# Kernel optimization log

Measured on AMD Instinct MI355X. Metric: run time of the kernel, lower is better.

The kernel has to match this reference:

```python
import jax, jax.numpy as jnp
import numpy as np

H = 2048      # hidden_dim
DI = 4096     # intermediate_size
N = 128       # state_size
NH = 64       # num_heads
P = 64        # head_dim
K = 4         # conv kernel
CH = 256      # chunk size
L = 4096      # seq len
DT_MIN, DT_MAX = 1e-3, 1e2


def setup_inputs() -> dict:
    key = jax.random.key(0)
    ks = jax.random.split(key, 8)
    conv_dim = DI + 2 * N
    x = jax.random.normal(ks[0], (L, H), jnp.float32)
    W_in = jax.random.normal(ks[1], (DI + 2 * N + NH, H), jnp.float32) / np.sqrt(H)
    conv_w = jax.random.normal(ks[2], (conv_dim, 1, K), jnp.float32) / np.sqrt(K)
    conv_b = jax.random.normal(ks[3], (conv_dim,), jnp.float32) * 0.01
    u = jax.random.uniform(ks[4], (NH,))
    dt = jnp.exp(u * (np.log(0.1) - np.log(0.001)) + np.log(0.001))
    dt = jnp.maximum(dt, 1e-4)
    dt_bias = dt + jnp.log(-jnp.expm1(-dt))   # inverse-softplus init
    A_log = jnp.log(jax.random.uniform(ks[5], (NH,), minval=1.0, maxval=16.0))
    D = jnp.ones((NH,), jnp.float32)
    norm_w = jnp.ones((DI,), jnp.float32)
    W_out = jax.random.normal(ks[6], (H, DI), jnp.float32) / np.sqrt(DI)
    return dict(x=x, W_in=W_in, conv_w=conv_w, conv_b=conv_b, dt_bias=dt_bias,
                A_log=A_log, D=D, norm_w=norm_w, W_out=W_out)


def _causal_decay(a):
    # a: [..., T] per-step log-decays -> exp(segment sum) as lower-tri [..., T, T]
    T = a.shape[-1]
    strict = jnp.tril(jnp.ones((T, T), bool), -1)
    full = jnp.tril(jnp.ones((T, T), bool), 0)
    s = jnp.cumsum(jnp.where(strict, a[..., None], 0.0), axis=-2)
    return jnp.where(full, jnp.exp(s), 0.0)


def reference(x, W_in, conv_w, conv_b, dt_bias, A_log, D, norm_w, W_out):
    conv_dim = DI + 2 * N
    xBCdt = x @ W_in.T                                  # [L, DI+2N+NH]
    xBC, dt = xBCdt[:, :conv_dim], xBCdt[:, conv_dim:]
    # causal depthwise conv1d + SiLU
    z = jax.lax.conv_general_dilated(
        xBC.T[None], conv_w, (1,), [(K - 1, 0)],
        dimension_numbers=('NCH', 'OIH', 'NCH'),
        feature_group_count=conv_dim)[0] + conv_b[:, None]
    xBC = jax.nn.silu(z.T)                              # [L, conv_dim]
    x_ssm = xBC[:, :DI].reshape(L, NH, P)
    Bm = xBC[:, DI:DI + N]                              # [L, N] shared over heads
    Cm = xBC[:, DI + N:]                                # [L, N]
    dt = jnp.clip(jax.nn.softplus(dt + dt_bias), DT_MIN, DT_MAX)  # [L, NH]
    A = -jnp.exp(A_log.astype(jnp.float32))             # [NH]
    dA = dt * A                                         # [L, NH]
    xdt = x_ssm * dt[:, :, None]                        # [L, NH, P]
    nc = L // CH
    xc = xdt.reshape(nc, CH, NH, P)
    Bc = Bm.reshape(nc, CH, N)
    Cc = Cm.reshape(nc, CH, N)
    dAc = dA.reshape(nc, CH, NH)
    A_cs = jnp.cumsum(dAc, axis=1)                      # [c, k, h]
    # intra-chunk (diagonal blocks)
    Lmat = _causal_decay(dAc.transpose(0, 2, 1))        # [c, h, k, k]
    Y_diag = jnp.einsum('ckn,csn,chks,cshp->ckhp', Cc, Bc, Lmat, xc)
    # per-chunk right states
    decay_states = jnp.exp(A_cs[:, -1:, :] - A_cs)      # [c, k, h]
    states = jnp.einsum('ckn,ckh,ckhp->chpn', Bc, decay_states, xc)
    # inter-chunk recurrence (no initial state)
    chunk_sum = A_cs[:, -1, :].T                        # [h, c]
    dec = _causal_decay(jnp.pad(chunk_sum, ((0, 0), (1, 0))))  # [h, c+1, c+1]
    states = jnp.concatenate([jnp.zeros((1, NH, P, N), states.dtype), states], 0)
    new_states = jnp.einsum('hzc,chpn->zhpn', dec, states)      # [c+1, h, p, n]
    prev = new_states[:-1]                              # [c, h, p, n]
    Y_off = jnp.einsum('ckn,chpn,ckh->ckhp', Cc, prev, jnp.exp(A_cs))
    Y = (Y_diag + Y_off).reshape(L, NH, P) + x_ssm * D[None, :, None]
    y = Y.reshape(L, DI)
    # RMSNorm
    var = jnp.mean(jnp.square(y.astype(jnp.float32)), -1, keepdims=True)
    y = (y * jax.lax.rsqrt(var + 1e-6)) * norm_w
    return y @ W_out.T
```

## Files before the change

### kernel.cpp

```cpp
#include <hip/hip_runtime.h>


typedef __bf16 bf16;
typedef __bf16 bf16x8 __attribute__((ext_vector_type(8)));
typedef __bf16 bf16x4 __attribute__((ext_vector_type(4)));
typedef float  f32x4  __attribute__((ext_vector_type(4)));

#define DEV static __device__ __forceinline__

DEV f32x4 mfma16(bf16x8 a, bf16x8 b, f32x4 c) {
  return __builtin_amdgcn_mfma_f32_16x16x32_bf16(a, b, c, 0, 0, 0);
}

DEV void gll16(const bf16* g, bf16* l) {
  __builtin_amdgcn_global_load_lds(
      (const __attribute__((address_space(1))) unsigned int*)g,
      (__attribute__((address_space(3))) unsigned int*)l, 16, 0, 0);
}

#define BAR()   asm volatile("s_barrier" ::: "memory")
#define VMW(n)  asm volatile("s_waitcnt vmcnt(" #n ")" ::: "memory")

template <int NT, int LD, bool DTC>
__global__ __launch_bounds__(512) void gemm_kernel(
    const bf16* __restrict__ Abase, const bf16* __restrict__ Bbase,
    bf16* __restrict__ C0, bf16* __restrict__ C1,
    float* __restrict__ dt0, float* __restrict__ dt1, int ldc, int ntN) {
  __shared__ __align__(16) bf16 lds[2 * 32768];
  const int tid = threadIdx.x;
  const int wid = tid >> 6, lane = tid & 63;
  const int lrow = lane & 15;
  const int colb = (lane >> 4) * 16;
  const int xorv = (lrow & 7) << 4;
  const int wm = wid & 1, wn = wid >> 1;
  const int bx = blockIdx.x / ntN, by = blockIdx.x % ntN;
  const int row0 = bx * 256, col0 = by * 256;
  const bf16* A = Abase + (size_t)blockIdx.y * (NT * 64);
  const bf16* B = Bbase + (size_t)blockIdx.y * (NT * 64);
  bf16* C = blockIdx.y ? C1 : C0;

  const int P = tid * 16;
  const int Lc = P ^ (((P >> 7) & 7) << 4);
  const int srow = Lc >> 7;
  const int selem = (Lc & 127) >> 1;
  const bf16* gA[4];
  const bf16* gB[4];
#pragma unroll
  for (int q = 0; q < 4; ++q) {
    gA[q] = A + (size_t)(row0 + q * 64 + srow) * LD + selem;
    gB[q] = B + (size_t)(col0 + q * 64 + srow) * LD + selem;
  }
  auto stage = [&](int s, int ko) {
#pragma unroll
    for (int q = 0; q < 4; ++q)
      gll16(gA[q] + ko, lds + s * 32768 + q * 4096 + tid * 8);
#pragma unroll
    for (int q = 0; q < 4; ++q)
      gll16(gB[q] + ko, lds + s * 32768 + 16384 + q * 4096 + tid * 8);
  };
  auto rdA = [&](int s, int m, int ks) -> bf16x8 {
    int row = wm * 128 + m * 16 + lrow;
    int cb = ((ks << 6) | colb) ^ xorv;
    return *(const bf16x8*)((const char*)(lds + s * 32768) + row * 128 + cb);
  };
  auto rdB = [&](int s, int n, int ks) -> bf16x8 {
    int row = wn * 64 + n * 16 + lrow;
    int cb = ((ks << 6) | colb) ^ xorv;
    return *(const bf16x8*)((const char*)(lds + s * 32768 + 16384) + row * 128 + cb);
  };

  f32x4 acc[8][4] = {};
  bf16x8 aF[4][2], bF[4][2];

  stage(0, 0);
  VMW(0);
  BAR();

  for (int t = 0; t < NT; ++t) {
    const int s = t & 1;
    if (t + 1 < NT) stage(s ^ 1, (t + 1) * 64);
#pragma unroll
    for (int n = 0; n < 4; ++n)
#pragma unroll
      for (int ks = 0; ks < 2; ++ks) bF[n][ks] = rdB(s, n, ks);
#pragma unroll
    for (int m = 0; m < 4; ++m)
#pragma unroll
      for (int ks = 0; ks < 2; ++ks) aF[m][ks] = rdA(s, m, ks);
#pragma unroll
    for (int m = 0; m < 4; ++m)
#pragma unroll
      for (int n = 0; n < 4; ++n)
#pragma unroll
        for (int ks = 0; ks < 2; ++ks)
          acc[m][n] = mfma16(aF[m][ks], bF[n][ks], acc[m][n]);
#pragma unroll
    for (int m = 0; m < 4; ++m)
#pragma unroll
      for (int ks = 0; ks < 2; ++ks) aF[m][ks] = rdA(s, m + 4, ks);
#pragma unroll
    for (int m = 0; m < 4; ++m)
#pragma unroll
      for (int n = 0; n < 4; ++n)
#pragma unroll
        for (int ks = 0; ks < 2; ++ks)
          acc[m + 4][n] = mfma16(aF[m][ks], bF[n][ks], acc[m + 4][n]);
    if (t + 1 < NT) {
      VMW(0);
      BAR();
    }
  }
  const int orow = (lane >> 4) * 4;
#pragma unroll
  for (int m = 0; m < 8; ++m)
#pragma unroll
    for (int n = 0; n < 4; ++n)
#pragma unroll
      for (int i = 0; i < 4; ++i) {
        int r = row0 + wm * 128 + m * 16 + orow + i;
        int c = col0 + wn * 64 + n * 16 + lrow;
        C[(size_t)r * ldc + c] = (bf16)acc[m][n][i];
      }
  if (DTC && by == 17 && wn == 0) {
    float* dtp = blockIdx.y ? dt1 : dt0;
#pragma unroll
    for (int m = 0; m < 8; ++m)
#pragma unroll
      for (int n = 0; n < 4; ++n)
#pragma unroll
        for (int i = 0; i < 4; ++i) {
          int r = row0 + wm * 128 + m * 16 + orow + i;
          int h = n * 16 + lrow;
          dtp[(size_t)r * 64 + h] = acc[m][n][i];
        }
  }
}

__global__ __launch_bounds__(256) void add2b_kernel(
    const bf16* __restrict__ a, const bf16* __restrict__ b,
    float* __restrict__ o, long n8) {
  long i = (long)blockIdx.x * blockDim.x + threadIdx.x;
  long stride = (long)gridDim.x * blockDim.x;
  for (; i < n8; i += stride) {
    bf16x8 va = ((const bf16x8*)a)[i];
    bf16x8 vb = ((const bf16x8*)b)[i];
    float4 o0, o1;
    o0.x = (float)va[0] + (float)vb[0];
    o0.y = (float)va[1] + (float)vb[1];
    o0.z = (float)va[2] + (float)vb[2];
    o0.w = (float)va[3] + (float)vb[3];
    o1.x = (float)va[4] + (float)vb[4];
    o1.y = (float)va[5] + (float)vb[5];
    o1.z = (float)va[6] + (float)vb[6];
    o1.w = (float)va[7] + (float)vb[7];
    ((float4*)o)[i * 2] = o0;
    ((float4*)o)[i * 2 + 1] = o1;
  }
}

__global__ __launch_bounds__(256) void cast_f2b_kernel(
    const float* __restrict__ in, bf16* __restrict__ out, long n4) {
  long i = (long)blockIdx.x * blockDim.x + threadIdx.x;
  long stride = (long)gridDim.x * blockDim.x;
  for (; i < n4; i += stride) {
    float4 v = ((const float4*)in)[i];
    bf16x4 o = {(bf16)v.x, (bf16)v.y, (bf16)v.z, (bf16)v.w};
    ((bf16x4*)out)[i] = o;
  }
}

__global__ __launch_bounds__(256) void cast_pad_kernel(
    const float* __restrict__ in, bf16* __restrict__ out, long n4, long valid4) {
  long i = (long)blockIdx.x * blockDim.x + threadIdx.x;
  long stride = (long)gridDim.x * blockDim.x;
  for (; i < n4; i += stride) {
    bf16x4 o = {(bf16)0.f, (bf16)0.f, (bf16)0.f, (bf16)0.f};
    if (i < valid4) {
      float4 v = ((const float4*)in)[i];
      o = bf16x4{(bf16)v.x, (bf16)v.y, (bf16)v.z, (bf16)v.w};
    }
    ((bf16x4*)out)[i] = o;
  }
}

__global__ __launch_bounds__(256) void dt_scan_kernel(
    const float* __restrict__ dt0, const float* __restrict__ dt1,
    const float* __restrict__ dt_bias, const float* __restrict__ A_log,
    float* __restrict__ dt, float* __restrict__ Acs, float* __restrict__ decayO,
    float* __restrict__ expAcs, float* __restrict__ csum) {
  const int c = blockIdx.x, h = blockIdx.y;
  const int k = threadIdx.x;
  const int t = c * 256 + k;
  __shared__ float buf[256];
  size_t idx = (size_t)t * 64 + h;
  float raw = dt0[idx] + dt1[idx] + dt_bias[h];
  float dtv = raw > 20.f ? raw : log1pf(__expf(raw));
  dtv = fminf(fmaxf(dtv, 0.001f), 100.f);
  dt[(size_t)t * 64 + h] = dtv;
  float dA = -__expf(A_log[h]) * dtv;
  buf[k] = dA;
  __syncthreads();
  for (int off = 1; off < 256; off <<= 1) {
    float add = (k >= off) ? buf[k - off] : 0.f;
    __syncthreads();
    buf[k] += add;
    __syncthreads();
  }
  float v = buf[k];
  float total = buf[255];
  size_t base = (size_t)(c * 64 + h) * 256 + k;
  Acs[base] = v;
  expAcs[base] = __expf(v);
  decayO[base] = __expf(total - v);
  if (k == 0) csum[c * 64 + h] = total;
}

__global__ __launch_bounds__(256) void conv_kernel(
    const bf16* __restrict__ xp0, const bf16* __restrict__ xp1,
    const float* __restrict__ conv_w, const float* __restrict__ conv_b,
    const float* __restrict__ dt, bf16* __restrict__ XS,
    bf16* __restrict__ XDT_T, bf16* __restrict__ Bm, bf16* __restrict__ BT,
    bf16* __restrict__ Cm) {
  const int t0 = blockIdx.x * 64;
  const int c0 = blockIdx.y * 64;
  __shared__ float lin[67 * 64];
  __shared__ bf16 tr[64 * 72];
  const int tid = threadIdx.x;
  for (int idx = tid; idx < 67 * 64; idx += 256) {
    int r = idx >> 6, cc = idx & 63;
    int gt = t0 + r - 3;
    size_t g = (size_t)gt * 4608 + c0 + cc;
    lin[idx] = (gt >= 0) ? ((float)xp0[g] + (float)xp1[g]) : 0.f;
  }
  __syncthreads();
  const int cl = tid & 63, tg = tid >> 6;
  const int ch = c0 + cl;
  const float w0 = conv_w[ch * 4 + 0], w1 = conv_w[ch * 4 + 1];
  const float w2 = conv_w[ch * 4 + 2], w3 = conv_w[ch * 4 + 3];
  const float bb = conv_b[ch];
  float vals[16];
  for (int j = 0; j < 16; ++j) {
    int tl = tg * 16 + j;
    float s = bb + lin[tl * 64 + cl] * w0 + lin[(tl + 1) * 64 + cl] * w1 +
              lin[(tl + 2) * 64 + cl] * w2 + lin[(tl + 3) * 64 + cl] * w3;
    vals[j] = s / (1.f + __expf(-s));
  }
  if (c0 < 4096) {
    const int hh = c0 >> 6;
    for (int j = 0; j < 16; ++j) {
      int t = t0 + tg * 16 + j;
      XS[(size_t)t * 4096 + ch] = (bf16)vals[j];
    }
    __syncthreads();
    for (int j = 0; j < 16; ++j) {
      int tl = tg * 16 + j;
      float dtv = dt[(size_t)(t0 + tl) * 64 + hh];
      tr[cl * 72 + tl] = (bf16)(vals[j] * dtv);
    }
    __syncthreads();
    int p = tid >> 2, toff = (tid & 3) * 16;
    bf16* dst = XDT_T + (size_t)(hh * 64 + p) * 4096 + t0 + toff;
    *(bf16x8*)(dst) = *(const bf16x8*)(tr + p * 72 + toff);
    *(bf16x8*)(dst + 8) = *(const bf16x8*)(tr + p * 72 + toff + 8);
  } else if (c0 < 4224) {
    const int n0 = c0 - 4096;
    for (int j = 0; j < 16; ++j) {
      int t = t0 + tg * 16 + j;
      Bm[(size_t)t * 128 + n0 + cl] = (bf16)vals[j];
    }
    __syncthreads();
    for (int j = 0; j < 16; ++j) tr[cl * 72 + tg * 16 + j] = (bf16)vals[j];
    __syncthreads();
    int p = tid >> 2, toff = (tid & 3) * 16;
    bf16* dst = BT + (size_t)(n0 + p) * 4096 + t0 + toff;
    *(bf16x8*)(dst) = *(const bf16x8*)(tr + p * 72 + toff);
    *(bf16x8*)(dst + 8) = *(const bf16x8*)(tr + p * 72 + toff + 8);
  } else {
    const int n0 = c0 - 4224;
    for (int j = 0; j < 16; ++j) {
      int t = t0 + tg * 16 + j;
      Cm[(size_t)t * 128 + n0 + cl] = (bf16)vals[j];
    }
  }
}

__global__ __launch_bounds__(256) void gmat_kernel(
    const bf16* __restrict__ Cm, const bf16* __restrict__ Bm,
    float* __restrict__ G) {
  const int c = blockIdx.x, kt = blockIdx.y, st = blockIdx.z;
  const int tid = threadIdx.x;
  const int wave = tid >> 6, lane = tid & 63;
  const int lrow = lane & 15, lk = (lane >> 4) * 8;
  const int wr = (wave >> 1) * 64, wc = (wave & 1) * 64;
  f32x4 acc[4][4] = {};
  for (int kk = 0; kk < 4; ++kk) {
    bf16x8 aF[4], bF[4];
    for (int m = 0; m < 4; ++m)
      aF[m] = *(const bf16x8*)(Cm + (size_t)(c * 256 + kt * 128 + wr + m * 16 + lrow) * 128 + kk * 32 + lk);
    for (int n = 0; n < 4; ++n)
      bF[n] = *(const bf16x8*)(Bm + (size_t)(c * 256 + st * 128 + wc + n * 16 + lrow) * 128 + kk * 32 + lk);
    for (int m = 0; m < 4; ++m)
      for (int n = 0; n < 4; ++n)
        acc[m][n] = mfma16(aF[m], bF[n], acc[m][n]);
  }
  const int orow = (lane >> 4) * 4;
  for (int m = 0; m < 4; ++m)
    for (int n = 0; n < 4; ++n)
      for (int i = 0; i < 4; ++i) {
        int k = kt * 128 + wr + m * 16 + orow + i;
        int s = st * 128 + wc + n * 16 + lrow;
        G[((size_t)c * 256 + k) * 256 + s] = acc[m][n][i];
      }
}

__global__ __launch_bounds__(256) void states_kernel(
    const bf16* __restrict__ XDT_T, const bf16* __restrict__ BT,
    const float* __restrict__ decayO, float* __restrict__ states) {
  const int c = blockIdx.x, h = blockIdx.y;
  __shared__ bf16 Ap[64 * 264];
  __shared__ float sDec[256];
  const int tid = threadIdx.x;
  const int wave = tid >> 6, lane = tid & 63;
  const int lrow = lane & 15, lk = (lane >> 4) * 8;
  sDec[tid] = decayO[(size_t)(c * 64 + h) * 256 + tid];
  __syncthreads();
  {
    int p = tid >> 2, kb = (tid & 3) * 64;
    const bf16* src = XDT_T + (size_t)(h * 64 + p) * 4096 + c * 256 + kb;
    for (int j = 0; j < 8; ++j) {
      bf16x8 v = *(const bf16x8*)(src + j * 8);
      bf16x8 o;
      for (int i = 0; i < 8; ++i) o[i] = (bf16)((float)v[i] * sDec[kb + j * 8 + i]);
      *(bf16x8*)(Ap + p * 264 + kb + j * 8) = o;
    }
  }
  __syncthreads();
  const int nb = wave * 32;
  f32x4 acc[4][2] = {};
  for (int kk = 0; kk < 8; ++kk) {
    bf16x8 aF[4], bF[2];
    for (int m = 0; m < 4; ++m)
      aF[m] = *(const bf16x8*)(Ap + (m * 16 + lrow) * 264 + kk * 32 + lk);
    for (int n = 0; n < 2; ++n)
      bF[n] = *(const bf16x8*)(BT + (size_t)(nb + n * 16 + lrow) * 4096 + c * 256 + kk * 32 + lk);
    for (int m = 0; m < 4; ++m)
      for (int n = 0; n < 2; ++n)
        acc[m][n] = mfma16(aF[m], bF[n], acc[m][n]);
  }
  float* st = states + (size_t)(c * 64 + h) * 64 * 128;
  const int orow = (lane >> 4) * 4;
  for (int m = 0; m < 4; ++m)
    for (int n = 0; n < 2; ++n)
      for (int i = 0; i < 4; ++i)
        st[(size_t)(m * 16 + orow + i) * 128 + nb + n * 16 + lrow] = acc[m][n][i];
}

__global__ __launch_bounds__(128) void chunk_rec_kernel(
    const float* __restrict__ states, const float* __restrict__ csum,
    bf16* __restrict__ prev) {
  const int h = blockIdx.x, p = blockIdx.y;
  const int n = threadIdx.x;
  size_t base = (size_t)h * 64 * 128 + (size_t)p * 128 + n;
  float run = 0.f;
  for (int c = 0; c < 16; ++c) {
    size_t idx = (size_t)c * 64 * 64 * 128 + base;
    prev[idx] = (bf16)run;
    run = run * __expf(csum[c * 64 + h]) + states[idx];
  }
}

__global__ __launch_bounds__(256) void ydiag_kernel(
    const bf16* __restrict__ Cm, const bf16* __restrict__ prev,
    const float* __restrict__ G, const float* __restrict__ Acs,
    const float* __restrict__ expAcs, const bf16* __restrict__ XDT_T,
    const bf16* __restrict__ XS, const float* __restrict__ Dp,
    float* __restrict__ Y) {
  const int c = blockIdx.x, h = blockIdx.y;
  __shared__ float sAcs[256];
  __shared__ float sExp[256];
  __shared__ __align__(16) bf16 pv[64 * 136];
  __shared__ __align__(16) bf16 xd[64 * 264];
  const int tid = threadIdx.x;
  const int wave = tid >> 6, lane = tid & 63;
  const int lrow = lane & 15, lk = (lane >> 4) * 8;
  const int wv16 = wave * 16;
  sAcs[tid] = Acs[(size_t)(c * 64 + h) * 256 + tid];
  sExp[tid] = expAcs[(size_t)(c * 64 + h) * 256 + tid];
  {
    int r = tid >> 2, q = (tid & 3) * 32;
    const bf16* src = prev + (size_t)(c * 64 + h) * 8192 + r * 128 + q;
    bf16* dst = pv + r * 136 + q;
    for (int j = 0; j < 4; ++j)
      *(bf16x8*)(dst + j * 8) = *(const bf16x8*)(src + j * 8);
  }
  {
    int r = tid >> 2, q = (tid & 3) * 64;
    const bf16* src = XDT_T + (size_t)(h * 64 + r) * 4096 + c * 256 + q;
    bf16* dst = xd + r * 264 + q;
    for (int j = 0; j < 8; ++j)
      *(bf16x8*)(dst + j * 8) = *(const bf16x8*)(src + j * 8);
  }
  __syncthreads();
  f32x4 acc[4][4] = {};
  __builtin_amdgcn_s_setprio(1);
  for (int kk = 0; kk < 4; ++kk) {
    bf16x8 aF[4], bF[4];
    for (int m = 0; m < 4; ++m)
      aF[m] = *(const bf16x8*)(Cm + (size_t)(c * 256 + m * 64 + wv16 + lrow) * 128 + kk * 32 + lk);
    for (int n = 0; n < 4; ++n)
      bF[n] = *(const bf16x8*)(pv + (n * 16 + lrow) * 136 + kk * 32 + lk);
    for (int m = 0; m < 4; ++m)
      for (int n = 0; n < 4; ++n)
        acc[m][n] = mfma16(aF[m], bF[n], acc[m][n]);
  }
  __builtin_amdgcn_s_setprio(0);
  const int orow = (lane >> 4) * 4;
  for (int m = 0; m < 4; ++m)
    for (int i = 0; i < 4; ++i) {
      float e = sExp[m * 64 + wv16 + orow + i];
      for (int n = 0; n < 4; ++n) acc[m][n][i] *= e;
    }
  const float* Gp = G + (size_t)c * 65536;
  for (int stile = 0; stile < 4; ++stile) {
    const int s0 = stile * 64;
    for (int kk = 0; kk < 2; ++kk) {
      bf16x8 bF[4];
      for (int n = 0; n < 4; ++n)
        bF[n] = *(const bf16x8*)(xd + (n * 16 + lrow) * 264 + s0 + kk * 32 + lk);
      for (int m = 0; m < 4; ++m) {
        if (m * 64 + wv16 + 15 < s0) continue;
        const int row = m * 64 + wv16 + lrow;
        const float ak = sAcs[row];
        const float* grow = Gp + (size_t)row * 256 + s0 + kk * 32 + lk;
        bf16x8 af;
        for (int j = 0; j < 8; ++j) {
          int s = s0 + kk * 32 + lk + j;
          float v = grow[j] * __expf(ak - sAcs[s]);
          if (s > row) v = 0.f;
          af[j] = (bf16)v;
        }
        __builtin_amdgcn_s_setprio(1);
        for (int n = 0; n < 4; ++n)
          acc[m][n] = mfma16(af, bF[n], acc[m][n]);
        __builtin_amdgcn_s_setprio(0);
      }
    }
  }
  const float Dh = Dp[h];
  for (int m = 0; m < 4; ++m)
    for (int n = 0; n < 4; ++n)
      for (int i = 0; i < 4; ++i) {
        int t = c * 256 + m * 64 + wv16 + orow + i;
        int col = h * 64 + n * 16 + lrow;
        float xs = (float)XS[(size_t)t * 4096 + col];
        Y[(size_t)t * 4096 + col] = acc[m][n][i] + xs * Dh;
      }
}

__global__ __launch_bounds__(256) void rmsnorm_kernel(
    const float* __restrict__ Y, const float* __restrict__ norm_w,
    bf16* __restrict__ out) {
  const int row = blockIdx.x;
  const float4* y4 = (const float4*)(Y + (size_t)row * 4096);
  float4 v[4];
  float ss = 0.f;
  for (int j = 0; j < 4; ++j) {
    v[j] = y4[threadIdx.x + j * 256];
    ss += v[j].x * v[j].x + v[j].y * v[j].y + v[j].z * v[j].z + v[j].w * v[j].w;
  }
  for (int off = 32; off; off >>= 1) ss += __shfl_down(ss, off, 64);
  __shared__ float ws[4];
  if ((threadIdx.x & 63) == 0) ws[threadIdx.x >> 6] = ss;
  __syncthreads();
  float scale = rsqrtf((ws[0] + ws[1] + ws[2] + ws[3]) / 4096.f + 1e-6f);
  for (int j = 0; j < 4; ++j) {
    int col = (threadIdx.x + j * 256) * 4;
    float4 w = *(const float4*)(norm_w + col);
    bf16x4 o = {(bf16)(v[j].x * scale * w.x), (bf16)(v[j].y * scale * w.y),
                (bf16)(v[j].z * scale * w.z), (bf16)(v[j].w * scale * w.w)};
    *(bf16x4*)(out + (size_t)row * 4096 + col) = o;
  }
}

extern "C" void kernel_launch(void* const* d_in, const int* in_sizes, int n_in,
                              void* d_out, int out_size, void* d_ws, size_t ws_size,
                              hipStream_t stream) {
  const float* x       = (const float*)d_in[0];
  const float* W_in    = (const float*)d_in[1];
  const float* conv_w  = (const float*)d_in[2];
  const float* conv_b  = (const float*)d_in[3];
  const float* dt_bias = (const float*)d_in[4];
  const float* A_log   = (const float*)d_in[5];
  const float* Dp      = (const float*)d_in[6];
  const float* norm_w  = (const float*)d_in[7];
  const float* W_out   = (const float*)d_in[8];

  size_t o = 0;
  char* base = (char*)d_ws;
  auto take = [&](size_t b) {
    char* p = base + o;
    o += (b + 255) & ~(size_t)255;
    return (void*)p;
  };
  bf16*  xb     = (bf16*)take((size_t)4096 * 2048 * 2);
  bf16*  winb   = (bf16*)take((size_t)4608 * 2048 * 2);
  bf16*  xp0b   = (bf16*)take((size_t)4096 * 4608 * 2);
  bf16*  xp1b   = (bf16*)take((size_t)4096 * 4608 * 2);
  float* dt0    = (float*)take((size_t)4096 * 64 * 4);
  float* dt1    = (float*)take((size_t)4096 * 64 * 4);
  float* dtg    = (float*)take((size_t)4096 * 64 * 4);
  float* Acs    = (float*)take((size_t)4096 * 64 * 4);
  float* decayO = (float*)take((size_t)4096 * 64 * 4);
  float* expA   = (float*)take((size_t)4096 * 64 * 4);
  float* csum   = (float*)take((size_t)16 * 64 * 4);
  bf16*  XS     = (bf16*)take((size_t)4096 * 4096 * 2);
  bf16*  XDT_T  = (bf16*)take((size_t)4096 * 4096 * 2);
  bf16*  Bm     = (bf16*)take((size_t)4096 * 128 * 2);
  bf16*  BT     = (bf16*)take((size_t)4096 * 128 * 2);
  bf16*  Cm     = (bf16*)take((size_t)4096 * 128 * 2);
  float* Y      = (float*)take((size_t)4096 * 4096 * 4);
  float* G      = (float*)((char*)xp0b);
  float* states = (float*)((char*)xp0b + (size_t)4194304);
  bf16*  prev   = (bf16*)((char*)xp0b + (size_t)37748736);
  bf16*  woutb  = (bf16*)((char*)xp0b + (size_t)54525952);
  bf16*  ynorm  = xb;
  bf16*  p2a    = XS;
  bf16*  p2b    = XDT_T;

  cast_f2b_kernel<<<2048, 256, 0, stream>>>(x, xb, (long)4096 * 2048 / 4);
  cast_pad_kernel<<<2048, 256, 0, stream>>>(W_in, winb, (long)4608 * 2048 / 4,
                                            (long)4416 * 2048 / 4);
  gemm_kernel<16, 2048, true><<<dim3(288, 2), 512, 0, stream>>>(
      xb, winb, xp0b, xp1b, dt0, dt1, 4608, 18);
  dt_scan_kernel<<<dim3(16, 64), 256, 0, stream>>>(dt0, dt1, dt_bias, A_log,
                                                   dtg, Acs, decayO, expA, csum);
  conv_kernel<<<dim3(64, 68), 256, 0, stream>>>(xp0b, xp1b, conv_w, conv_b, dtg,
                                                XS, XDT_T, Bm, BT, Cm);
  gmat_kernel<<<dim3(16, 2, 2), 256, 0, stream>>>(Cm, Bm, G);
  states_kernel<<<dim3(16, 64), 256, 0, stream>>>(XDT_T, BT, decayO, states);
  chunk_rec_kernel<<<dim3(64, 64), 128, 0, stream>>>(states, csum, prev);
  cast_f2b_kernel<<<2048, 256, 0, stream>>>(W_out, woutb, (long)2048 * 4096 / 4);
  ydiag_kernel<<<dim3(16, 64), 256, 0, stream>>>(Cm, prev, G, Acs, expA, XDT_T,
                                                 XS, Dp, Y);
  rmsnorm_kernel<<<4096, 256, 0, stream>>>(Y, norm_w, ynorm);
  gemm_kernel<32, 4096, false><<<dim3(128, 2), 512, 0, stream>>>(
      ynorm, woutb, p2a, p2b, nullptr, nullptr, 2048, 8);
  add2b_kernel<<<2048, 256, 0, stream>>>(p2a, p2b, (float*)d_out,
                                         (long)4096 * 2048 / 8);
}
```

Before: 375.7 us.

## Triple-buffer GEMM with BK=32, store G in bf16, move D-skip into RMSNorm

```diff
diff --git a/kernel.cpp b/kernel.cpp
--- a/kernel.cpp
+++ b/kernel.cpp
@@ -26,91 +26,68 @@
     const bf16* __restrict__ Abase, const bf16* __restrict__ Bbase,
     bf16* __restrict__ C0, bf16* __restrict__ C1,
     float* __restrict__ dt0, float* __restrict__ dt1, int ldc, int ntN) {
-  __shared__ __align__(16) bf16 lds[2 * 32768];
+  __shared__ __align__(16) bf16 lds[3 * 16384];
   const int tid = threadIdx.x;
   const int wid = tid >> 6, lane = tid & 63;
   const int lrow = lane & 15;
-  const int colb = (lane >> 4) * 16;
-  const int xorv = (lrow & 7) << 4;
+  const int lc = lane >> 4;
   const int wm = wid & 1, wn = wid >> 1;
   const int bx = blockIdx.x / ntN, by = blockIdx.x % ntN;
   const int row0 = bx * 256, col0 = by * 256;
-  const bf16* A = Abase + (size_t)blockIdx.y * (NT * 64);
-  const bf16* B = Bbase + (size_t)blockIdx.y * (NT * 64);
+  const bf16* A = Abase + (size_t)blockIdx.y * (NT * 32);
+  const bf16* B = Bbase + (size_t)blockIdx.y * (NT * 32);
   bf16* C = blockIdx.y ? C1 : C0;
 
-  const int P = tid * 16;
-  const int Lc = P ^ (((P >> 7) & 7) << 4);
-  const int srow = Lc >> 7;
-  const int selem = (Lc & 127) >> 1;
-  const bf16* gA[4];
-  const bf16* gB[4];
-#pragma unroll
-  for (int q = 0; q < 4; ++q) {
-    gA[q] = A + (size_t)(row0 + q * 64 + srow) * LD + selem;
-    gB[q] = B + (size_t)(col0 + q * 64 + srow) * LD + selem;
+  const bf16* gA[2];
+  const bf16* gB[2];
+#pragma unroll
+  for (int q = 0; q < 2; ++q) {
+    int P = q * 8192 + tid * 16;
+    int Bq = P ^ (((P >> 7) & 3) << 4);
+    int srow = Bq >> 6;
+    int selem = (Bq & 63) >> 1;
+    gA[q] = A + (size_t)(row0 + srow) * LD + selem;
+    gB[q] = B + (size_t)(col0 + srow) * LD + selem;
   }
   auto stage = [&](int s, int ko) {
-#pragma unroll
-    for (int q = 0; q < 4; ++q)
-      gll16(gA[q] + ko, lds + s * 32768 + q * 4096 + tid * 8);
-#pragma unroll
-    for (int q = 0; q < 4; ++q)
-      gll16(gB[q] + ko, lds + s * 32768 + 16384 + q * 4096 + tid * 8);
+    bf16* sl = lds + s * 16384;
+    gll16(gA[0] + ko, sl + tid * 8);
+    gll16(gA[1] + ko, sl + 4096 + tid * 8);
+    gll16(gB[0] + ko, sl + 8192 + tid * 8);
+    gll16(gB[1] + ko, sl + 12288 + tid * 8);
   };
-  auto rdA = [&](int s, int m, int ks) -> bf16x8 {
+  auto rdA = [&](int s, int m) -> bf16x8 {
     int row = wm * 128 + m * 16 + lrow;
-    int cb = ((ks << 6) | colb) ^ xorv;
-    return *(const bf16x8*)((const char*)(lds + s * 32768) + row * 128 + cb);
+    int off = row * 64 + ((lc ^ ((row >> 1) & 3)) << 4);
+    return *(const bf16x8*)((const char*)(lds + s * 16384) + off);
   };
-  auto rdB = [&](int s, int n, int ks) -> bf16x8 {
+  auto rdB = [&](int s, int n) -> bf16x8 {
     int row = wn * 64 + n * 16 + lrow;
-    int cb = ((ks << 6) | colb) ^ xorv;
-    return *(const bf16x8*)((const char*)(lds + s * 32768 + 16384) + row * 128 + cb);
+    int off = row * 64 + ((lc ^ ((row >> 1) & 3)) << 4);
+    return *(const bf16x8*)((const char*)(lds + s * 16384) + 16384 + off);
   };
 
   f32x4 acc[8][4] = {};
-  bf16x8 aF[4][2], bF[4][2];
-
   stage(0, 0);
-  VMW(0);
-  BAR();
-
+  stage(1, 32);
+  int rs = 0, ws = 2;
   for (int t = 0; t < NT; ++t) {
-    const int s = t & 1;
-    if (t + 1 < NT) stage(s ^ 1, (t + 1) * 64);
-#pragma unroll
-    for (int n = 0; n < 4; ++n)
-#pragma unroll
-      for (int ks = 0; ks < 2; ++ks) bF[n][ks] = rdB(s, n, ks);
-#pragma unroll
-    for (int m = 0; m < 4; ++m)
-#pragma unroll
-      for (int ks = 0; ks < 2; ++ks) aF[m][ks] = rdA(s, m, ks);
-#pragma unroll
-    for (int m = 0; m < 4; ++m)
-#pragma unroll
-      for (int n = 0; n < 4; ++n)
-#pragma unroll
-        for (int ks = 0; ks < 2; ++ks)
-          acc[m][n] = mfma16(aF[m][ks], bF[n][ks], acc[m][n]);
-#pragma unroll
-    for (int m = 0; m < 4; ++m)
-#pragma unroll
-      for (int ks = 0; ks < 2; ++ks) aF[m][ks] = rdA(s, m + 4, ks);
-#pragma unroll
-    for (int m = 0; m < 4; ++m)
-#pragma unroll
-      for (int n = 0; n < 4; ++n)
-#pragma unroll
-        for (int ks = 0; ks < 2; ++ks)
-          acc[m + 4][n] = mfma16(aF[m][ks], bF[n][ks], acc[m + 4][n]);
-    if (t + 1 < NT) {
-      VMW(0);
-      BAR();
-    }
-  }
-  const int orow = (lane >> 4) * 4;
+    if (t + 1 < NT) { VMW(4); } else { VMW(0); }
+    BAR();
+    if (t + 2 < NT) stage(ws, (t + 2) * 32);
+    bf16x8 b0 = rdB(rs, 0), b1 = rdB(rs, 1), b2 = rdB(rs, 2), b3 = rdB(rs, 3);
+#pragma unroll
+    for (int m = 0; m < 8; ++m) {
+      bf16x8 a = rdA(rs, m);
+      acc[m][0] = mfma16(a, b0, acc[m][0]);
+      acc[m][1] = mfma16(a, b1, acc[m][1]);
+      acc[m][2] = mfma16(a, b2, acc[m][2]);
+      acc[m][3] = mfma16(a, b3, acc[m][3]);
+    }
+    rs = (rs == 2) ? 0 : rs + 1;
+    ws = (ws == 2) ? 0 : ws + 1;
+  }
+  const int orow = lc * 4;
 #pragma unroll
   for (int m = 0; m < 8; ++m)
 #pragma unroll
@@ -286,7 +263,7 @@
 
 __global__ __launch_bounds__(256) void gmat_kernel(
     const bf16* __restrict__ Cm, const bf16* __restrict__ Bm,
-    float* __restrict__ G) {
+    bf16* __restrict__ G) {
   const int c = blockIdx.x, kt = blockIdx.y, st = blockIdx.z;
   const int tid = threadIdx.x;
   const int wave = tid >> 6, lane = tid & 63;
@@ -309,7 +286,7 @@
       for (int i = 0; i < 4; ++i) {
         int k = kt * 128 + wr + m * 16 + orow + i;
         int s = st * 128 + wc + n * 16 + lrow;
-        G[((size_t)c * 256 + k) * 256 + s] = acc[m][n][i];
+        G[((size_t)c * 256 + k) * 256 + s] = (bf16)acc[m][n][i];
       }
 }
 
@@ -371,9 +348,8 @@
 
 __global__ __launch_bounds__(256) void ydiag_kernel(
     const bf16* __restrict__ Cm, const bf16* __restrict__ prev,
-    const float* __restrict__ G, const float* __restrict__ Acs,
+    const bf16* __restrict__ Gb, const float* __restrict__ Acs,
     const float* __restrict__ expAcs, const bf16* __restrict__ XDT_T,
-    const bf16* __restrict__ XS, const float* __restrict__ Dp,
     float* __restrict__ Y) {
   const int c = blockIdx.x, h = blockIdx.y;
   __shared__ float sAcs[256];
@@ -402,71 +378,103 @@
   }
   __syncthreads();
   f32x4 acc[4][4] = {};
-  __builtin_amdgcn_s_setprio(1);
+  bf16x8 aYo[4][4];
+#pragma unroll
+  for (int kk = 0; kk < 4; ++kk)
+#pragma unroll
+    for (int m = 0; m < 4; ++m)
+      aYo[kk][m] = *(const bf16x8*)(Cm + (size_t)(c * 256 + m * 64 + wv16 + lrow) * 128 + kk * 32 + lk);
+#pragma unroll
   for (int kk = 0; kk < 4; ++kk) {
-    bf16x8 aF[4], bF[4];
-    for (int m = 0; m < 4; ++m)
-      aF[m] = *(const bf16x8*)(Cm + (size_t)(c * 256 + m * 64 + wv16 + lrow) * 128 + kk * 32 + lk);
+    bf16x8 bF[4];
+#pragma unroll
     for (int n = 0; n < 4; ++n)
       bF[n] = *(const bf16x8*)(pv + (n * 16 + lrow) * 136 + kk * 32 + lk);
+#pragma unroll
     for (int m = 0; m < 4; ++m)
+#pragma unroll
       for (int n = 0; n < 4; ++n)
-        acc[m][n] = mfma16(aF[m], bF[n], acc[m][n]);
-  }
-  __builtin_amdgcn_s_setprio(0);
+        acc[m][n] = mfma16(aYo[kk][m], bF[n], acc[m][n]);
+  }
   const int orow = (lane >> 4) * 4;
+#pragma unroll
   for (int m = 0; m < 4; ++m)
+#pragma unroll
     for (int i = 0; i < 4; ++i) {
       float e = sExp[m * 64 + wv16 + orow + i];
       for (int n = 0; n < 4; ++n) acc[m][n][i] *= e;
     }
-  const float* Gp = G + (size_t)c * 65536;
+  const bf16* Gp = Gb + (size_t)c * 65536;
+#pragma unroll
   for (int stile = 0; stile < 4; ++stile) {
     const int s0 = stile * 64;
-    for (int kk = 0; kk < 2; ++kk) {
-      bf16x8 bF[4];
+    bf16x8 graw[2][4];
+#pragma unroll
+    for (int kk = 0; kk < 2; ++kk)
+#pragma unroll
+      for (int m = 0; m < 4; ++m)
+        if (m * 64 + wv16 + 15 >= s0) {
+          int row = m * 64 + wv16 + lrow;
+          graw[kk][m] = *(const bf16x8*)(Gp + (size_t)row * 256 + s0 + kk * 32 + lk);
+        }
+    bf16x8 bF[2][4];
+#pragma unroll
+    for (int kk = 0; kk < 2; ++kk)
+#pragma unroll
       for (int n = 0; n < 4; ++n)
-        bF[n] = *(const bf16x8*)(xd + (n * 16 + lrow) * 264 + s0 + kk * 32 + lk);
+        bF[kk][n] = *(const bf16x8*)(xd + (n * 16 + lrow) * 264 + s0 + kk * 32 + lk);
+#pragma unroll
+    for (int kk = 0; kk < 2; ++kk)
+#pragma unroll
       for (int m = 0; m < 4; ++m) {
         if (m * 64 + wv16 + 15 < s0) continue;
         const int row = m * 64 + wv16 + lrow;
         const float ak = sAcs[row];
-        const float* grow = Gp + (size_t)row * 256 + s0 + kk * 32 + lk;
         bf16x8 af;
+#pragma unroll
         for (int j = 0; j < 8; ++j) {
           int s = s0 + kk * 32 + lk + j;
-          float v = grow[j] * __expf(ak - sAcs[s]);
+          float v = (float)graw[kk][m][j] * __expf(ak - sAcs[s]);
           if (s > row) v = 0.f;
           af[j] = (bf16)v;
         }
-        __builtin_amdgcn_s_setprio(1);
+#pragma unroll
         for (int n = 0; n < 4; ++n)
-          acc[m][n] = mfma16(af, bF[n], acc[m][n]);
-        __builtin_amdgcn_s_setprio(0);
+          acc[m][n] = mfma16(af, bF[kk][n], acc[m][n]);
       }
-    }
-  }
-  const float Dh = Dp[h];
+  }
+#pragma unroll
   for (int m = 0; m < 4; ++m)
+#pragma unroll
     for (int n = 0; n < 4; ++n)
+#pragma unroll
       for (int i = 0; i < 4; ++i) {
         int t = c * 256 + m * 64 + wv16 + orow + i;
         int col = h * 64 + n * 16 + lrow;
-        float xs = (float)XS[(size_t)t * 4096 + col];
-        Y[(size_t)t * 4096 + col] = acc[m][n][i] + xs * Dh;
+        Y[(size_t)t * 4096 + col] = acc[m][n][i];
       }
 }
 
 __global__ __launch_bounds__(256) void rmsnorm_kernel(
-    const float* __restrict__ Y, const float* __restrict__ norm_w,
+    const float* __restrict__ Y, const bf16* __restrict__ XS,
+    const float* __restrict__ Dp, const float* __restrict__ norm_w,
     bf16* __restrict__ out) {
   const int row = blockIdx.x;
   const float4* y4 = (const float4*)(Y + (size_t)row * 4096);
+  const bf16x4* xs4 = (const bf16x4*)(XS + (size_t)row * 4096);
   float4 v[4];
   float ss = 0.f;
   for (int j = 0; j < 4; ++j) {
-    v[j] = y4[threadIdx.x + j * 256];
-    ss += v[j].x * v[j].x + v[j].y * v[j].y + v[j].z * v[j].z + v[j].w * v[j].w;
+    int c4 = threadIdx.x + j * 256;
+    float4 y = y4[c4];
+    bf16x4 xs = xs4[c4];
+    float d = Dp[(c4 * 4) >> 6];
+    y.x += (float)xs[0] * d;
+    y.y += (float)xs[1] * d;
+    y.z += (float)xs[2] * d;
+    y.w += (float)xs[3] * d;
+    v[j] = y;
+    ss += y.x * y.x + y.y * y.y + y.z * y.z + y.w * y.w;
   }
   for (int off = 32; off; off >>= 1) ss += __shfl_down(ss, off, 64);
   __shared__ float ws[4];
@@ -519,7 +527,7 @@
   bf16*  BT     = (bf16*)take((size_t)4096 * 128 * 2);
   bf16*  Cm     = (bf16*)take((size_t)4096 * 128 * 2);
   float* Y      = (float*)take((size_t)4096 * 4096 * 4);
-  float* G      = (float*)((char*)xp0b);
+  bf16*  Gb     = (bf16*)((char*)xp0b);
   float* states = (float*)((char*)xp0b + (size_t)4194304);
   bf16*  prev   = (bf16*)((char*)xp0b + (size_t)37748736);
   bf16*  woutb  = (bf16*)((char*)xp0b + (size_t)54525952);
@@ -530,20 +538,20 @@
   cast_f2b_kernel<<<2048, 256, 0, stream>>>(x, xb, (long)4096 * 2048 / 4);
   cast_pad_kernel<<<2048, 256, 0, stream>>>(W_in, winb, (long)4608 * 2048 / 4,
                                             (long)4416 * 2048 / 4);
-  gemm_kernel<16, 2048, true><<<dim3(288, 2), 512, 0, stream>>>(
+  gemm_kernel<32, 2048, true><<<dim3(288, 2), 512, 0, stream>>>(
       xb, winb, xp0b, xp1b, dt0, dt1, 4608, 18);
   dt_scan_kernel<<<dim3(16, 64), 256, 0, stream>>>(dt0, dt1, dt_bias, A_log,
                                                    dtg, Acs, decayO, expA, csum);
   conv_kernel<<<dim3(64, 68), 256, 0, stream>>>(xp0b, xp1b, conv_w, conv_b, dtg,
                                                 XS, XDT_T, Bm, BT, Cm);
-  gmat_kernel<<<dim3(16, 2, 2), 256, 0, stream>>>(Cm, Bm, G);
+  gmat_kernel<<<dim3(16, 2, 2), 256, 0, stream>>>(Cm, Bm, Gb);
   states_kernel<<<dim3(16, 64), 256, 0, stream>>>(XDT_T, BT, decayO, states);
   chunk_rec_kernel<<<dim3(64, 64), 128, 0, stream>>>(states, csum, prev);
   cast_f2b_kernel<<<2048, 256, 0, stream>>>(W_out, woutb, (long)2048 * 4096 / 4);
-  ydiag_kernel<<<dim3(16, 64), 256, 0, stream>>>(Cm, prev, G, Acs, expA, XDT_T,
-                                                 XS, Dp, Y);
-  rmsnorm_kernel<<<4096, 256, 0, stream>>>(Y, norm_w, ynorm);
-  gemm_kernel<32, 4096, false><<<dim3(128, 2), 512, 0, stream>>>(
+  ydiag_kernel<<<dim3(16, 64), 256, 0, stream>>>(Cm, prev, Gb, Acs, expA,
+                                                 XDT_T, Y);
+  rmsnorm_kernel<<<4096, 256, 0, stream>>>(Y, XS, Dp, norm_w, ynorm);
+  gemm_kernel<64, 4096, false><<<dim3(128, 2), 512, 0, stream>>>(
       ynorm, woutb, p2a, p2b, nullptr, nullptr, 2048, 8);
   add2b_kernel<<<2048, 256, 0, stream>>>(p2a, p2b, (float*)d_out,
                                          (long)4096 * 2048 / 8);
```

After: 345.7 us. -8.0%, faster.
